# Optimization experiments

Hardware: AMD Instinct MI355X
Metric: run time of the kernel (lower is better)

## Reference

```python
import jax, jax.numpy as jnp
import numpy as np

N_DRUG = 25000
N_DIS = 25000
N = N_DRUG + N_DIS
E = 800000
D_IN = 128
D_OUT = 128


def setup_inputs() -> dict:
    key = jax.random.key(0)
    k1, k2, k3, k4, k5, k6 = jax.random.split(key, 6)
    drug_f = jax.random.normal(k1, (N_DRUG, D_IN), dtype=jnp.float32)
    disease_f = jax.random.normal(k2, (N_DIS, D_IN), dtype=jnp.float32)
    rows = jax.random.randint(k3, (E,), 0, N, dtype=jnp.int64)
    cols = jax.random.randint(k4, (E,), 0, N, dtype=jnp.int64)
    # xavier_uniform_ equivalent for [D_IN, D_OUT]
    limit = float(np.sqrt(6.0 / (D_IN + D_OUT)))
    drug_w = jax.random.uniform(k5, (D_IN, D_OUT), minval=-limit, maxval=limit, dtype=jnp.float32)
    disease_w = jax.random.uniform(k6, (D_IN, D_OUT), minval=-limit, maxval=limit, dtype=jnp.float32)
    return {"drug_f": drug_f, "disease_f": disease_f, "drug_w": drug_w,
            "disease_w": disease_w, "rows": rows, "cols": cols}


def reference(drug_f, disease_f, drug_w, disease_w, rows, cols):
    # per-type linear projection
    drug_h = drug_f @ drug_w          # [n_drug, D_OUT]
    dis_h = disease_f @ disease_w     # [n_dis,  D_OUT]
    node_f = jnp.concatenate([drug_h, dis_h], axis=0)  # [N, D_OUT]
    # row-sum degrees of the (unit-valued) sparse adjacency, clamped at 1
    deg = jax.ops.segment_sum(jnp.ones((rows.shape[0],), node_f.dtype), rows,
                              num_segments=N)
    norm = jnp.clip(deg, 1.0, None) ** -0.5           # [N]
    # symmetric norm: norm * (A @ (norm * x)); SpMM as gather + segment_sum
    node_f = node_f * norm[:, None]
    msgs = node_f[cols]                               # [E, D_OUT]
    node_f = jax.ops.segment_sum(msgs, rows, num_segments=N)
    node_f = node_f * norm[:, None]
    return node_f
```

## Files before the change

kernel.cpp:

```cpp
#include <hip/hip_runtime.h>
#include <hip/hip_bf16.h>

#define D 128
#define CAP 64
#define BINSH 7
#define NSHARD 8
#define NCHUNK 384
#define PART_EDGES 4096

typedef short short8 __attribute__((ext_vector_type(8)));
typedef unsigned short ushort8 __attribute__((ext_vector_type(8)));
typedef float f32x4  __attribute__((ext_vector_type(4)));

__device__ __forceinline__ short f2bf(float x) {
    __hip_bfloat16 b = __float2bfloat16(x);
    return *reinterpret_cast<short*>(&b);
}
__device__ __forceinline__ float bf2f(unsigned short u) {
    return __uint_as_float((unsigned)u << 16);
}

__device__ __forceinline__ void wprep_block(int b16, int tid,
                                            const float* __restrict__ w0,
                                            const float* __restrict__ w1,
                                            __hip_bfloat16* __restrict__ wb) {
    int gid = b16 * 256 + tid;
    int type = gid >> 11;
    int tri  = gid & 2047;
    int lane = tri & 63;
    int ts   = tri >> 6;
    int s = ts & 3, t = ts >> 2;
    const float* W = type ? w1 : w0;
    int n = t * 16 + (lane & 15);
    int kbase = s * 32 + (lane >> 4) * 8;
    short8 v;
    #pragma unroll
    for (int j = 0; j < 8; ++j)
        v[j] = f2bf(W[(size_t)(kbase + j) * D + n]);
    *(short8*)&wb[(size_t)type * 16384 + (size_t)tri * 8] = v;
}

__global__ __launch_bounds__(256) void prep_sort_kernel(const float* __restrict__ w0,
                                                        const float* __restrict__ w1,
                                                        __hip_bfloat16* __restrict__ wb,
                                                        int* __restrict__ bincur, int nbin) {
    int b = blockIdx.x;
    if (b < 16) { wprep_block(b, threadIdx.x, w0, w1, wb); return; }
    for (int i = threadIdx.x; i < nbin; i += 256) bincur[i] = 0;
}

__global__ __launch_bounds__(256) void part_proj_kernel(
    const int* __restrict__ rows, const int* __restrict__ cols,
    int* __restrict__ bincur, unsigned int* __restrict__ payload,
    int E, int nbin, int capbin, int nparts,
    const float* __restrict__ f0, const float* __restrict__ f1,
    const __hip_bfloat16* __restrict__ wb,
    __hip_bfloat16* __restrict__ h,
    int n0, int n1, int nb0) {

    __shared__ short8 Wl[2048];
    int b = blockIdx.x;
    int t = threadIdx.x;

    if (b < nparts) {
        int* hist = (int*)&Wl[0];
        int* base = hist + 512;
        int* cur  = hist + 1024;
        int lo = b * PART_EDGES;
        int hi = lo + PART_EDGES; if (hi > E) hi = E;

        for (int i = t; i < nbin; i += 256) hist[i] = 0;
        __syncthreads();
        for (int i = lo + t; i < hi; i += 256)
            atomicAdd(&hist[rows[i] >> BINSH], 1);
        __syncthreads();
        for (int i = t; i < nbin; i += 256) {
            int c = hist[i];
            base[i] = (c > 0) ? atomicAdd(&bincur[i], c) : 0;
            cur[i] = 0;
        }
        __syncthreads();
        for (int i = lo + t; i < hi; i += 256) {
            int r = rows[i];
            int bn = r >> BINSH;
            int p = base[bn] + atomicAdd(&cur[bn], 1);
            if (p < capbin)
                payload[(size_t)bn * capbin + p] = ((unsigned)r << 16) | (unsigned)(cols[i] & 0xffff);
        }
        return;
    }

    int pb = b - nparts;
    int type = (pb >= nb0) ? 1 : 0;
    const float* f = type ? f1 : f0;
    int lbase = (type ? (pb - nb0) : pb) * 64;
    int nloc  = type ? n1 : n0;
    int goff  = type ? n0 : 0;

    const short8* src = (const short8*)wb + (size_t)type * 2048;
    for (int i = t; i < 2048; i += 256) Wl[i] = src[i];
    __syncthreads();

    int wave = t >> 6;
    int lane = t & 63;
    int m  = lane & 15;
    int kg = lane >> 4;
    int wrow = lbase + wave * 16;

    int arow = wrow + m;
    int arc = (arow < nloc) ? arow : (nloc - 1);
    const float* fr = f + (size_t)arc * D + kg * 8;
    short8 A[4];
    #pragma unroll
    for (int s = 0; s < 4; ++s) {
        float4 x = *(const float4*)(fr + s * 32);
        float4 y = *(const float4*)(fr + s * 32 + 4);
        short8 a;
        a[0] = f2bf(x.x); a[1] = f2bf(x.y); a[2] = f2bf(x.z); a[3] = f2bf(x.w);
        a[4] = f2bf(y.x); a[5] = f2bf(y.y); a[6] = f2bf(y.z); a[7] = f2bf(y.w);
        A[s] = a;
    }

    #pragma unroll
    for (int tt = 0; tt < 8; ++tt) {
        f32x4 acc = {0.f, 0.f, 0.f, 0.f};
        #pragma unroll
        for (int s = 0; s < 4; ++s)
            acc = __builtin_amdgcn_mfma_f32_16x16x32_bf16(A[s], Wl[(tt * 4 + s) * 64 + lane], acc, 0, 0, 0);
        #pragma unroll
        for (int r = 0; r < 4; ++r) {
            int grow = wrow + kg * 4 + r;
            if (grow < nloc)
                h[(size_t)(goff + grow) * D + tt * 16 + m] = __float2bfloat16(acc[r]);
        }
    }
}

__global__ __launch_bounds__(256) void binfill_kernel(const unsigned int* __restrict__ payload,
                                                      const int* __restrict__ bincur,
                                                      unsigned short* __restrict__ bucket,
                                                      int* __restrict__ cnt,
                                                      float* __restrict__ normf,
                                                      int capbin, int N) {
    __shared__ int rc[128];
    int b = blockIdx.x;
    int t = threadIdx.x;
    if (t < 128) rc[t] = 0;
    __syncthreads();
    int cntb = bincur[b]; if (cntb > capbin) cntb = capbin;
    const unsigned int* pp = payload + (size_t)b * capbin;
    for (int i = t; i < cntb; i += 256) {
        unsigned pay = pp[i];
        int rl = (pay >> 16) & 127;
        int p = atomicAdd(&rc[rl], 1);
        if (p < CAP)
            bucket[(size_t)((b << BINSH) | rl) * CAP + p] = (unsigned short)(pay & 0xffff);
    }
    __syncthreads();
    if (t < 128) {
        int r = (b << BINSH) | t;
        if (r < N) {
            int c = rc[t];
            cnt[r] = c;
            normf[r] = rsqrtf((float)(c < 1 ? 1 : c));
        }
    }
}

__global__ __launch_bounds__(256) void agg_kernel(const int* __restrict__ cnt,
                                                  const float* __restrict__ normf,
                                                  const unsigned short* __restrict__ bucket,
                                                  const __hip_bfloat16* __restrict__ h,
                                                  float* __restrict__ out, int n) {
    int wave = threadIdx.x >> 6;
    int lane = threadIdx.x & 63;
    int r = blockIdx.x * 4 + wave;
    if (r >= n) return;
    int d = cnt[r]; if (d > CAP) d = CAP;
    int s = r * CAP;

    int col = (int)bucket[s + lane];
    int cs  = (lane < d) ? col : 0;
    float wl = (lane < d) ? normf[cs] : 0.f;

    int g  = lane >> 4;
    int sl = lane & 15;

    float acc[8] = {0.f,0.f,0.f,0.f,0.f,0.f,0.f,0.f};
    int j = 0;
    for (; j + 8 <= d; j += 8) {
        int e0 = j + g, e1 = j + 4 + g;
        float w0 = __shfl(wl, e0);
        float w1 = __shfl(wl, e1);
        int   c0 = __shfl(cs, e0);
        int   c1 = __shfl(cs, e1);
        ushort8 v0 = *(const ushort8*)&h[(size_t)c0 * D + sl * 8];
        ushort8 v1 = *(const ushort8*)&h[(size_t)c1 * D + sl * 8];
        #pragma unroll
        for (int k = 0; k < 8; ++k)
            acc[k] += w0 * bf2f(v0[k]) + w1 * bf2f(v1[k]);
    }
    for (; j < d; j += 4) {
        int e = j + g;
        float we = __shfl(wl, e & 63); if (e >= d) we = 0.f;
        int   ce = __shfl(cs, e & 63);
        ushort8 v = *(const ushort8*)&h[(size_t)ce * D + sl * 8];
        #pragma unroll
        for (int k = 0; k < 8; ++k)
            acc[k] += we * bf2f(v[k]);
    }
    #pragma unroll
    for (int k = 0; k < 8; ++k) {
        acc[k] += __shfl_xor(acc[k], 16);
        acc[k] += __shfl_xor(acc[k], 32);
    }
    if (g == 0) {
        float nr = normf[r];
        float* po = &out[(size_t)r * D + sl * 8];
        *(float4*)po       = make_float4(acc[0]*nr, acc[1]*nr, acc[2]*nr, acc[3]*nr);
        *(float4*)(po + 4) = make_float4(acc[4]*nr, acc[5]*nr, acc[6]*nr, acc[7]*nr);
    }
}

__global__ __launch_bounds__(256) void prep_kernel(const float* __restrict__ w0,
                                                   const float* __restrict__ w1,
                                                   __hip_bfloat16* __restrict__ wb,
                                                   int* __restrict__ cnt, int N) {
    int b = blockIdx.x;
    if (b < 16) { wprep_block(b, threadIdx.x, w0, w1, wb); }
    else {
        int i = (b - 16) * 256 + threadIdx.x;
        if (i < N) cnt[i] = 0;
    }
}

__global__ __launch_bounds__(256) void fill_shard_kernel(const int* __restrict__ rows,
                                                         const int* __restrict__ cols,
                                                         int* __restrict__ cnt,
                                                         unsigned short* __restrict__ bucket,
                                                         int E, int shsz, int ch) {
    int s     = blockIdx.x & (NSHARD - 1);
    int chunk = blockIdx.x >> 3;
    int lo = chunk * ch;
    int hi = lo + ch; if (hi > E) hi = E;
    int rlo = s * shsz;
    for (int i = lo + (int)threadIdx.x; i < hi; i += 256) {
        int r = rows[i];
        if ((unsigned)(r - rlo) < (unsigned)shsz) {
            int p = atomicAdd(&cnt[r], 1);
            if (p < CAP) bucket[(size_t)r * CAP + p] = (unsigned short)cols[i];
        }
    }
}

__global__ void norm_from_cnt_kernel(const int* __restrict__ cnt, float* __restrict__ normf, int N) {
    int i = blockIdx.x * 256 + threadIdx.x;
    if (i < N) { int c = cnt[i]; normf[i] = rsqrtf((float)(c < 1 ? 1 : c)); }
}

extern "C" void kernel_launch(void* const* d_in, const int* in_sizes, int n_in,
                              void* d_out, int out_size, void* d_ws, size_t ws_size,
                              hipStream_t stream) {
    const float* drug_f    = (const float*)d_in[0];
    const float* disease_f = (const float*)d_in[1];
    const float* drug_w    = (const float*)d_in[2];
    const float* disease_w = (const float*)d_in[3];
    const int*   rows      = (const int*)d_in[4];
    const int*   cols      = (const int*)d_in[5];
    float* out = (float*)d_out;

    int n_drug = in_sizes[0] / D;
    int n_dis  = in_sizes[1] / D;
    int N = n_drug + n_dis;
    int E = in_sizes[4];
    (void)out_size; (void)n_in;

    char* ws = (char*)d_ws;
    size_t off = 0;
    auto alloc = [&](size_t bytes) { void* p = ws + off; off = (off + bytes + 255) & ~(size_t)255; return p; };

    int*            cnt      = (int*)alloc(sizeof(int) * N);
    float*          normf    = (float*)alloc(sizeof(float) * N);
    __hip_bfloat16* h_raw    = (__hip_bfloat16*)alloc(sizeof(__hip_bfloat16) * (size_t)N * D);
    __hip_bfloat16* wb       = (__hip_bfloat16*)alloc(sizeof(__hip_bfloat16) * 2 * 16384);
    unsigned short* bucket   = (unsigned short*)alloc((size_t)N * CAP * sizeof(unsigned short));

    int nb0 = (n_drug + 63) / 64;
    int nb1 = (n_dis + 63) / 64;

    int nbin   = (N + (1 << BINSH) - 1) >> BINSH;
    int capbin = (((E / nbin) * 3 / 2) + 63) & ~63;
    size_t sort_need = off
        + ((sizeof(int) * nbin + 255) & ~(size_t)255)
        + ((sizeof(unsigned int) * (size_t)nbin * capbin + 255) & ~(size_t)255);

    if (ws_size >= sort_need && nbin <= 512) {
        int*          bincur  = (int*)alloc(sizeof(int) * nbin);
        unsigned int* payload = (unsigned int*)alloc(sizeof(unsigned int) * (size_t)nbin * capbin);

        int nparts = (E + PART_EDGES - 1) / PART_EDGES;
        prep_sort_kernel<<<17, 256, 0, stream>>>(drug_w, disease_w, wb, bincur, nbin);
        part_proj_kernel<<<nparts + nb0 + nb1, 256, 0, stream>>>(
            rows, cols, bincur, payload, E, nbin, capbin, nparts,
            drug_f, disease_f, wb, h_raw, n_drug, n_dis, nb0);
        binfill_kernel<<<nbin, 256, 0, stream>>>(payload, bincur, bucket, cnt, normf, capbin, N);
        agg_kernel<<<(N + 3) / 4, 256, 0, stream>>>(cnt, normf, bucket, h_raw, out, N);
    } else {
        int shsz = (N + NSHARD - 1) / NSHARD;
        int ch   = (E + NCHUNK - 1) / NCHUNK;
        int prep_blocks = 16 + (N + 255) / 256;

        prep_kernel<<<prep_blocks, 256, 0, stream>>>(drug_w, disease_w, wb, cnt, N);
        fill_shard_kernel<<<NCHUNK * NSHARD, 256, 0, stream>>>(rows, cols, cnt, bucket, E, shsz, ch);
        norm_from_cnt_kernel<<<(N + 255) / 256, 256, 0, stream>>>(cnt, normf, N);
        part_proj_kernel<<<nb0 + nb1, 256, 0, stream>>>(
            rows, cols, (int*)nullptr, (unsigned int*)nullptr, E, nbin, capbin, 0,
            drug_f, disease_f, wb, h_raw, n_drug, n_dis, nb0);
        agg_kernel<<<(N + 3) / 4, 256, 0, stream>>>(cnt, normf, bucket, h_raw, out, N);
    }
}
```

Measured before the change: 69.48 us.

## Drop global bin counters and weight prep kernel; use per-partition segments

Removes the separate prep kernel by converting weights to bf16 MFMA layout inside each projection block, and replaces the global atomic bin-offset scheme with per-(bin, partition) fixed-capacity segments plus a counts table. Each partition block now scatters in a single pass with only shared-memory atomics, and binfill walks one segment per thread. This saves one kernel launch, a histogram pass and the global atomics. In exchange every projection block re-reads and converts the fp32 weights, and binfill processes each segment serially in one thread, which may be slow. Overflow beyond capseg per segment drops edges.

```diff
diff --git a/kernel.cpp b/kernel.cpp
--- a/kernel.cpp
+++ b/kernel.cpp
@@ -6,7 +6,6 @@
 #define BINSH 7
 #define NSHARD 8
 #define NCHUNK 384
-#define PART_EDGES 4096
 
 typedef short short8 __attribute__((ext_vector_type(8)));
 typedef unsigned short ushort8 __attribute__((ext_vector_type(8)));
@@ -20,41 +19,12 @@
     return __uint_as_float((unsigned)u << 16);
 }
 
-__device__ __forceinline__ void wprep_block(int b16, int tid,
-                                            const float* __restrict__ w0,
-                                            const float* __restrict__ w1,
-                                            __hip_bfloat16* __restrict__ wb) {
-    int gid = b16 * 256 + tid;
-    int type = gid >> 11;
-    int tri  = gid & 2047;
-    int lane = tri & 63;
-    int ts   = tri >> 6;
-    int s = ts & 3, t = ts >> 2;
-    const float* W = type ? w1 : w0;
-    int n = t * 16 + (lane & 15);
-    int kbase = s * 32 + (lane >> 4) * 8;
-    short8 v;
-    #pragma unroll
-    for (int j = 0; j < 8; ++j)
-        v[j] = f2bf(W[(size_t)(kbase + j) * D + n]);
-    *(short8*)&wb[(size_t)type * 16384 + (size_t)tri * 8] = v;
-}
-
-__global__ __launch_bounds__(256) void prep_sort_kernel(const float* __restrict__ w0,
-                                                        const float* __restrict__ w1,
-                                                        __hip_bfloat16* __restrict__ wb,
-                                                        int* __restrict__ bincur, int nbin) {
-    int b = blockIdx.x;
-    if (b < 16) { wprep_block(b, threadIdx.x, w0, w1, wb); return; }
-    for (int i = threadIdx.x; i < nbin; i += 256) bincur[i] = 0;
-}
-
 __global__ __launch_bounds__(256) void part_proj_kernel(
     const int* __restrict__ rows, const int* __restrict__ cols,
-    int* __restrict__ bincur, unsigned int* __restrict__ payload,
-    int E, int nbin, int capbin, int nparts,
+    int* __restrict__ counts, unsigned int* __restrict__ payload,
+    int E, int nbin, int nparts, int pe, int capseg,
     const float* __restrict__ f0, const float* __restrict__ f1,
-    const __hip_bfloat16* __restrict__ wb,
+    const float* __restrict__ w0, const float* __restrict__ w1,
     __hip_bfloat16* __restrict__ h,
     int n0, int n1, int nb0) {
 
@@ -63,29 +33,24 @@
     int t = threadIdx.x;
 
     if (b < nparts) {
-        int* hist = (int*)&Wl[0];
-        int* base = hist + 512;
-        int* cur  = hist + 1024;
-        int lo = b * PART_EDGES;
-        int hi = lo + PART_EDGES; if (hi > E) hi = E;
-
-        for (int i = t; i < nbin; i += 256) hist[i] = 0;
+        int* cur = (int*)&Wl[0];
+        for (int i = t; i < nbin; i += 256) cur[i] = 0;
         __syncthreads();
-        for (int i = lo + t; i < hi; i += 256)
-            atomicAdd(&hist[rows[i] >> BINSH], 1);
+        int lo = b * pe;
+        int hi = lo + pe; if (hi > E) hi = E;
+        for (int i = lo + t; i < hi; i += 256) {
+            int r = rows[i];
+            int c = cols[i];
+            int bn = r >> BINSH;
+            int p = atomicAdd(&cur[bn], 1);
+            if (p < capseg)
+                payload[((size_t)bn * nparts + b) * capseg + p] =
+                    ((unsigned)r << 16) | (unsigned)(c & 0xffff);
+        }
         __syncthreads();
         for (int i = t; i < nbin; i += 256) {
-            int c = hist[i];
-            base[i] = (c > 0) ? atomicAdd(&bincur[i], c) : 0;
-            cur[i] = 0;
-        }
-        __syncthreads();
-        for (int i = lo + t; i < hi; i += 256) {
-            int r = rows[i];
-            int bn = r >> BINSH;
-            int p = base[bn] + atomicAdd(&cur[bn], 1);
-            if (p < capbin)
-                payload[(size_t)bn * capbin + p] = ((unsigned)r << 16) | (unsigned)(cols[i] & 0xffff);
+            int c = cur[i]; if (c > capseg) c = capseg;
+            counts[(size_t)i * nparts + b] = c;
         }
         return;
     }
@@ -93,12 +58,22 @@
     int pb = b - nparts;
     int type = (pb >= nb0) ? 1 : 0;
     const float* f = type ? f1 : f0;
+    const float* W = type ? w1 : w0;
     int lbase = (type ? (pb - nb0) : pb) * 64;
     int nloc  = type ? n1 : n0;
     int goff  = type ? n0 : 0;
 
-    const short8* src = (const short8*)wb + (size_t)type * 2048;
-    for (int i = t; i < 2048; i += 256) Wl[i] = src[i];
+    for (int i = t; i < 2048; i += 256) {
+        int lane = i & 63, ts = i >> 6;
+        int s = ts & 3, tt = ts >> 2;
+        int n = tt * 16 + (lane & 15);
+        int kbase = s * 32 + (lane >> 4) * 8;
+        short8 v;
+        #pragma unroll
+        for (int j = 0; j < 8; ++j)
+            v[j] = f2bf(W[(size_t)(kbase + j) * D + n]);
+        Wl[i] = v;
+    }
     __syncthreads();
 
     int wave = t >> 6;
@@ -137,24 +112,27 @@
 }
 
 __global__ __launch_bounds__(256) void binfill_kernel(const unsigned int* __restrict__ payload,
-                                                      const int* __restrict__ bincur,
+                                                      const int* __restrict__ counts,
                                                       unsigned short* __restrict__ bucket,
                                                       int* __restrict__ cnt,
                                                       float* __restrict__ normf,
-                                                      int capbin, int N) {
+                                                      int nparts, int capseg, int N) {
     __shared__ int rc[128];
     int b = blockIdx.x;
     int t = threadIdx.x;
     if (t < 128) rc[t] = 0;
     __syncthreads();
-    int cntb = bincur[b]; if (cntb > capbin) cntb = capbin;
-    const unsigned int* pp = payload + (size_t)b * capbin;
-    for (int i = t; i < cntb; i += 256) {
-        unsigned pay = pp[i];
-        int rl = (pay >> 16) & 127;
-        int p = atomicAdd(&rc[rl], 1);
-        if (p < CAP)
-            bucket[(size_t)((b << BINSH) | rl) * CAP + p] = (unsigned short)(pay & 0xffff);
+    if (t < nparts) {
+        int cntc = counts[(size_t)b * nparts + t];
+        if (cntc > capseg) cntc = capseg;
+        const unsigned int* seg = payload + ((size_t)b * nparts + t) * capseg;
+        for (int p = 0; p < cntc; ++p) {
+            unsigned pay = seg[p];
+            int rl = (pay >> 16) & 127;
+            int q = atomicAdd(&rc[rl], 1);
+            if (q < CAP)
+                bucket[(size_t)((b << BINSH) | rl) * CAP + q] = (unsigned short)(pay & 0xffff);
+        }
     }
     __syncthreads();
     if (t < 128) {
@@ -222,16 +200,9 @@
     }
 }
 
-__global__ __launch_bounds__(256) void prep_kernel(const float* __restrict__ w0,
-                                                   const float* __restrict__ w1,
-                                                   __hip_bfloat16* __restrict__ wb,
-                                                   int* __restrict__ cnt, int N) {
-    int b = blockIdx.x;
-    if (b < 16) { wprep_block(b, threadIdx.x, w0, w1, wb); }
-    else {
-        int i = (b - 16) * 256 + threadIdx.x;
-        if (i < N) cnt[i] = 0;
-    }
+__global__ void zero_cnt_kernel(int* __restrict__ cnt, int N) {
+    int i = blockIdx.x * 256 + threadIdx.x;
+    if (i < N) cnt[i] = 0;
 }
 
 __global__ __launch_bounds__(256) void fill_shard_kernel(const int* __restrict__ rows,
@@ -282,40 +253,41 @@
     int*            cnt      = (int*)alloc(sizeof(int) * N);
     float*          normf    = (float*)alloc(sizeof(float) * N);
     __hip_bfloat16* h_raw    = (__hip_bfloat16*)alloc(sizeof(__hip_bfloat16) * (size_t)N * D);
-    __hip_bfloat16* wb       = (__hip_bfloat16*)alloc(sizeof(__hip_bfloat16) * 2 * 16384);
     unsigned short* bucket   = (unsigned short*)alloc((size_t)N * CAP * sizeof(unsigned short));
 
     int nb0 = (n_drug + 63) / 64;
     int nb1 = (n_dis + 63) / 64;
 
-    int nbin   = (N + (1 << BINSH) - 1) >> BINSH;
-    int capbin = (((E / nbin) * 3 / 2) + 63) & ~63;
+    int nbin = (N + (1 << BINSH) - 1) >> BINSH;
+    int pe = (E + 255) / 256;
+    if (pe < 4096) pe = 4096;
+    int nparts = (E + pe - 1) / pe;
+    int capseg = ((pe / nbin) * 3 + 31) & ~15;
+
     size_t sort_need = off
-        + ((sizeof(int) * nbin + 255) & ~(size_t)255)
-        + ((sizeof(unsigned int) * (size_t)nbin * capbin + 255) & ~(size_t)255);
-
-    if (ws_size >= sort_need && nbin <= 512) {
-        int*          bincur  = (int*)alloc(sizeof(int) * nbin);
-        unsigned int* payload = (unsigned int*)alloc(sizeof(unsigned int) * (size_t)nbin * capbin);
-
-        int nparts = (E + PART_EDGES - 1) / PART_EDGES;
-        prep_sort_kernel<<<17, 256, 0, stream>>>(drug_w, disease_w, wb, bincur, nbin);
+        + ((sizeof(int) * (size_t)nbin * nparts + 255) & ~(size_t)255)
+        + ((sizeof(unsigned int) * (size_t)nbin * nparts * capseg + 255) & ~(size_t)255);
+
+    if (ws_size >= sort_need && nbin <= 512 && nparts <= 256) {
+        int*          counts  = (int*)alloc(sizeof(int) * (size_t)nbin * nparts);
+        unsigned int* payload = (unsigned int*)alloc(sizeof(unsigned int) * (size_t)nbin * nparts * capseg);
+
         part_proj_kernel<<<nparts + nb0 + nb1, 256, 0, stream>>>(
-            rows, cols, bincur, payload, E, nbin, capbin, nparts,
-            drug_f, disease_f, wb, h_raw, n_drug, n_dis, nb0);
-        binfill_kernel<<<nbin, 256, 0, stream>>>(payload, bincur, bucket, cnt, normf, capbin, N);
+            rows, cols, counts, payload, E, nbin, nparts, pe, capseg,
+            drug_f, disease_f, drug_w, disease_w, h_raw, n_drug, n_dis, nb0);
+        binfill_kernel<<<nbin, 256, 0, stream>>>(payload, counts, bucket, cnt, normf,
+                                                 nparts, capseg, N);
         agg_kernel<<<(N + 3) / 4, 256, 0, stream>>>(cnt, normf, bucket, h_raw, out, N);
     } else {
         int shsz = (N + NSHARD - 1) / NSHARD;
         int ch   = (E + NCHUNK - 1) / NCHUNK;
-        int prep_blocks = 16 + (N + 255) / 256;
-
-        prep_kernel<<<prep_blocks, 256, 0, stream>>>(drug_w, disease_w, wb, cnt, N);
+
+        zero_cnt_kernel<<<(N + 255) / 256, 256, 0, stream>>>(cnt, N);
         fill_shard_kernel<<<NCHUNK * NSHARD, 256, 0, stream>>>(rows, cols, cnt, bucket, E, shsz, ch);
         norm_from_cnt_kernel<<<(N + 255) / 256, 256, 0, stream>>>(cnt, normf, N);
         part_proj_kernel<<<nb0 + nb1, 256, 0, stream>>>(
-            rows, cols, (int*)nullptr, (unsigned int*)nullptr, E, nbin, capbin, 0,
-            drug_f, disease_f, wb, h_raw, n_drug, n_dis, nb0);
+            rows, cols, (int*)nullptr, (unsigned int*)nullptr, E, nbin, 0, pe, capseg,
+            drug_f, disease_f, drug_w, disease_w, h_raw, n_drug, n_dis, nb0);
         agg_kernel<<<(N + 3) / 4, 256, 0, stream>>>(cnt, normf, bucket, h_raw, out, N);
     }
 }
```

New measurement: 64.37 us. 7.4% less time.
